# Performance work log

Hardware: AMD Instinct MI355X
Metric: run time of the kernel (lower is better)

## Reference

```python
import jax, jax.numpy as jnp
import numpy as np

G = 256          # voxel grid extent per axis
N = 30000        # number of active voxels
CHANNELS = [(4,16),(16,16),(16,32),(32,32),(32,32),(32,64),(64,64),(64,64),(64,64),(64,64),(64,64),(64,64),(64,128)]
BN_EPS = 1e-3

_OFFS = np.array([[i, j, k] for i in (-1, 0, 1) for j in (-1, 0, 1) for k in (-1, 0, 1)], dtype=np.int32)  # 27 kernel taps


def setup_inputs() -> dict:
    key = jax.random.key(0)
    ks = jax.random.split(key, 2 + len(CHANNELS))
    rng = np.random.default_rng(0)
    # unique active voxel coordinates in [0, G)^3
    c = rng.integers(0, G, size=(2 * N, 3))
    c = np.unique(c, axis=0)
    rng.shuffle(c)
    coords = jnp.asarray(c[:N], dtype=jnp.int32)
    inp = {
        "voxel_features": jax.random.normal(ks[0], (N, CHANNELS[0][0]), jnp.float32),
        "coords": coords,
    }
    for i, (ci, co) in enumerate(CHANNELS):
        inp[f"W{i}"] = jax.random.normal(ks[1 + i], (27, ci, co), jnp.float32) * (1.0 / np.sqrt(27.0 * ci))
        inp[f"g{i}"] = jnp.ones((co,), jnp.float32)
        inp[f"b{i}"] = jnp.zeros((co,), jnp.float32)
    return inp


def _neighbors(coords):
    """Build rulebook: for each of 27 taps, index of neighbor voxel (or masked)."""
    n = coords.shape[0]
    grid = jnp.full((G, G, G), -1, jnp.int32).at[coords[:, 0], coords[:, 1], coords[:, 2]].set(
        jnp.arange(n, dtype=jnp.int32))
    offs = jnp.asarray(_OFFS)
    nc = coords[None, :, :] + offs[:, None, :]               # [27, N, 3]
    inb = jnp.all((nc >= 0) & (nc < G), axis=-1)             # [27, N]
    ncc = jnp.clip(nc, 0, G - 1)
    nidx = grid[ncc[..., 0], ncc[..., 1], ncc[..., 2]]       # [27, N]
    valid = (inb & (nidx >= 0)).astype(jnp.float32)
    return jnp.maximum(nidx, 0), valid


def _sconv(feat, W, nidx, valid):
    # gather-GEMM: gathered [27, N, Cin] -> out [N, Cout]
    g = feat[nidx] * valid[..., None]
    return jnp.einsum('knc,kcd->nd', g, W)


def _bn_relu(x, g, b):
    m = jnp.mean(x, axis=0)
    v = jnp.var(x, axis=0)
    return jax.nn.relu((x - m) * jax.lax.rsqrt(v + BN_EPS) * g + b)


def reference(voxel_features, coords,
              W0, W1, W2, W3, W4, W5, W6, W7, W8, W9, W10, W11, W12,
              g0, g1, g2, g3, g4, g5, g6, g7, g8, g9, g10, g11, g12,
              b0, b1, b2, b3, b4, b5, b6, b7, b8, b9, b10, b11, b12):
    Ws = [W0, W1, W2, W3, W4, W5, W6, W7, W8, W9, W10, W11, W12]
    gs = [g0, g1, g2, g3, g4, g5, g6, g7, g8, g9, g10, g11, g12]
    bs = [b0, b1, b2, b3, b4, b5, b6, b7, b8, b9, b10, b11, b12]
    nidx, valid = _neighbors(coords)
    x = voxel_features
    for W, g, b in zip(Ws, gs, bs):
        x = _bn_relu(_sconv(x, W, nidx, valid), g, b)
    return x  # [N, 128] final backbone features
```

## Files before the change

### kernel.cpp

```cpp
#include <hip/hip_runtime.h>
#include <stdint.h>
#include <stddef.h>

#define GG 256
#define STP 16

typedef __attribute__((ext_vector_type(8))) short bf16x8;
typedef __attribute__((ext_vector_type(4))) float f32x4;

__device__ __forceinline__ float bf2f(short s) {
  return __builtin_bit_cast(float, ((unsigned)(unsigned short)s) << 16);
}
__device__ __forceinline__ short f2bf(float f) {
  unsigned u = __builtin_bit_cast(unsigned, f);
  unsigned r = (u + 0x7FFFu + ((u >> 16) & 1u)) >> 16;
  return (short)r;
}


__global__ __launch_bounds__(256) void k_clear_grid(uint32_t* g, int n32) {
  int i = blockIdx.x * 256 + threadIdx.x;
  int stride = gridDim.x * 256;
  for (; i < n32; i += stride) g[i] = 0xFFFFFFFFu;
}

__global__ __launch_bounds__(256) void k_scatter(const int* __restrict__ coords,
                                                 uint16_t* __restrict__ grid, int n) {
  int i = blockIdx.x * 256 + threadIdx.x;
  if (i >= n) return;
  int x = coords[3 * i], y = coords[3 * i + 1], z = coords[3 * i + 2];
  grid[(((x << 8) | y) << 8) | z] = (uint16_t)i;
}

__global__ __launch_bounds__(256) void k_rulebook(const int* __restrict__ coords,
                                                  const uint16_t* __restrict__ grid,
                                                  short* __restrict__ nidx, int n) {
  int i = blockIdx.x * 256 + threadIdx.x;
  if (i >= n) return;
  int x = coords[3 * i], y = coords[3 * i + 1], z = coords[3 * i + 2];
  int k = 0;
  for (int dx = -1; dx <= 1; ++dx)
    for (int dy = -1; dy <= 1; ++dy)
      for (int dz = -1; dz <= 1; ++dz) {
        int nx = x + dx, ny = y + dy, nz = z + dz;
        short v = -1;
        if (((nx | ny | nz) >= 0) && nx < GG && ny < GG && nz < GG) {
          uint16_t s = grid[(((nx << 8) | ny) << 8) | nz];
          if (s != 0xFFFFu) v = (short)s;
        }
        nidx[k * n + i] = v;
        ++k;
      }
}


__global__ __launch_bounds__(256) void k_zero(float* __restrict__ stats, float* __restrict__ zp) {
  int tot = 13 * 256 * STP;
  for (int i = blockIdx.x * 256 + threadIdx.x; i < tot; i += gridDim.x * 256) stats[i] = 0.0f;
  if (blockIdx.x == 0 && threadIdx.x < 64) zp[threadIdx.x] = 0.0f;
}


struct PackArgs {
  const float* W[13];
  short* P[13];
  int ci[13], co[13], nkb[13];
};

__global__ __launch_bounds__(256) void k_pack(PackArgs pa) {
  int L = blockIdx.y;
  int ci = pa.ci[L], co = pa.co[L], nkb = pa.nkb[L];
  int total = nkb * co * 32;
  const float* W = pa.W[L];
  short* P = pa.P[L];
  for (int e = blockIdx.x * 256 + threadIdx.x; e < total; e += gridDim.x * 256) {
    int kk = e & 31;
    int rest = e >> 5;
    int c = rest % co;
    int kb = rest / co;
    int k = kb * 32 + kk;
    int tap = k / ci, cc = k % ci;
    float v = (tap < 27) ? W[((size_t)tap * ci + cc) * co + c] : 0.0f;
    P[e] = f2bf(v);
  }
}


__global__ __launch_bounds__(256) void k_sconv_l0(const float* __restrict__ feat,
                                                  const float* __restrict__ W,
                                                  const short* __restrict__ nidx,
                                                  float* __restrict__ y,
                                                  float* __restrict__ stats, int n) {
  int i = blockIdx.x * 256 + threadIdx.x;
  bool act = i < n;
  int ii = act ? i : (n - 1);
  float acc[16];
#pragma unroll
  for (int c = 0; c < 16; ++c) acc[c] = 0.0f;
  for (int t = 0; t < 27; ++t) {
    int nid = nidx[t * n + ii];
    float4 f = make_float4(0.f, 0.f, 0.f, 0.f);
    if (act && nid >= 0) f = *(const float4*)(feat + 4 * (size_t)nid);
    const float* Wt = W + t * 64;
#pragma unroll
    for (int c = 0; c < 16; ++c)
      acc[c] = fmaf(f.x, Wt[c],
               fmaf(f.y, Wt[16 + c],
               fmaf(f.z, Wt[32 + c],
               fmaf(f.w, Wt[48 + c], acc[c]))));
  }
  if (act) {
    float* o = y + (size_t)i * 16;
#pragma unroll
    for (int c = 0; c < 16; c += 4) *(float4*)(o + c) = make_float4(acc[c], acc[c+1], acc[c+2], acc[c+3]);
  }
  __shared__ float ss[4][16], sq[4][16];
  int w = threadIdx.x >> 6, l = threadIdx.x & 63;
#pragma unroll
  for (int c = 0; c < 16; ++c) {
    float s = act ? acc[c] : 0.0f;
    float q = s * s;
#pragma unroll
    for (int off = 32; off; off >>= 1) {
      s += __shfl_xor(s, off);
      q += __shfl_xor(q, off);
    }
    if (l == 0) { ss[w][c] = s; sq[w][c] = q; }
  }
  __syncthreads();
  if (threadIdx.x < 16) {
    int c = threadIdx.x;
    atomicAdd(&stats[c * STP], ss[0][c] + ss[1][c] + ss[2][c] + ss[3][c]);
    atomicAdd(&stats[(16 + c) * STP], sq[0][c] + sq[1][c] + sq[2][c] + sq[3][c]);
  }
}


template <int CI, int CO>
__global__ __launch_bounds__(256) void k_sconv_mfma(
    const short* __restrict__ feat, const short* __restrict__ P,
    const short* __restrict__ nidx, int zoff,
    float* __restrict__ y, int n) {
  constexpr int NKB = (27 * CI + 31) / 32;
  constexpr int MT = (CO == 16) ? 4 : (CO == 32) ? 2 : 1;
  constexpr int WPM = 4 / MT;
  constexpr int NT = CO / (16 * WPM);
  constexpr int R = MT * 16;
  constexpr int PF = 4;

  const int w = threadIdx.x >> 6;
  const int l = threadIdx.x & 63;
  const int lo = l & 15, g = l >> 4;
  const int mt = w / WPM, nw = w % WPM;
  const int bvox = blockIdx.x * R;
  const int rowg = bvox + mt * 16 + lo;
  const int rowc = (rowg < n) ? rowg : (n - 1);

  int offs[28];
#pragma unroll
  for (int t = 0; t < 27; ++t) {
    int nid = (int)nidx[t * n + rowc];
    offs[t] = (nid >= 0) ? nid * (CI * 2) : zoff;
  }
  offs[27] = zoff;

  const int chb0 = (CI == 16) ? ((g & 1) * 16) : (g * 16);
  const char* fb = (const char*)feat + chb0;

  const char* pb[NT];
#pragma unroll
  for (int j = 0; j < NT; ++j)
    pb[j] = (const char*)P + (((nw + j * WPM) * 16 + lo) * 64 + g * 16);

  auto A = [&](int kb) -> bf16x8 {
    int off;
    if (CI == 64) {
      off = offs[kb >> 1] + ((kb & 1) << 6);
    } else if (CI == 32) {
      off = offs[kb];
    } else {
      int o0 = offs[2 * kb];
      int o1 = offs[2 * kb + 1];
      off = (g < 2) ? o0 : o1;
    }
    return *(const bf16x8*)(fb + off);
  };

  bf16x8 ab[PF];
  bf16x8 bb[PF][NT];
#pragma unroll
  for (int i = 0; i < PF; ++i) {
    ab[i] = A(i);
#pragma unroll
    for (int j = 0; j < NT; ++j)
      bb[i][j] = *(const bf16x8*)(pb[j] + (size_t)i * (CO * 64));
  }

  f32x4 acc[NT];
#pragma unroll
  for (int j = 0; j < NT; ++j) acc[j] = (f32x4){0.f, 0.f, 0.f, 0.f};

#pragma unroll
  for (int kb = 0; kb < NKB; ++kb) {
    bf16x8 a = ab[kb % PF];
    bf16x8 bcur[NT];
#pragma unroll
    for (int j = 0; j < NT; ++j) bcur[j] = bb[kb % PF][j];
    if (kb + PF < NKB) {
      ab[kb % PF] = A(kb + PF);
#pragma unroll
      for (int j = 0; j < NT; ++j)
        bb[kb % PF][j] = *(const bf16x8*)(pb[j] + (size_t)(kb + PF) * (CO * 64));
    }
#pragma unroll
    for (int j = 0; j < NT; ++j)
      acc[j] = __builtin_amdgcn_mfma_f32_16x16x32_bf16(a, bcur[j], acc[j], 0, 0, 0);
  }

  __shared__ float ys[R * CO];
#pragma unroll
  for (int j = 0; j < NT; ++j) {
    int col = (nw + j * WPM) * 16 + lo;
#pragma unroll
    for (int r = 0; r < 4; ++r)
      ys[(mt * 16 + 4 * g + r) * CO + col] = acc[j][r];
  }
  __syncthreads();
  constexpr int IT = (R * CO / 4) / 256;
#pragma unroll
  for (int e4 = 0; e4 < IT; ++e4) {
    int e = e4 * 256 + threadIdx.x;
    int gidx = bvox * CO + e * 4;
    if (gidx < n * CO) *(float4*)(y + gidx) = *(const float4*)(ys + e * 4);
  }
}


template <int CO>
__global__ __launch_bounds__(256) void k_stats(const float* __restrict__ y,
                                               float* __restrict__ stats, int n) {
  const int tid = threadIdx.x;
  const int c0 = (tid * 4) & (CO - 1);
  float s0 = 0.f, s1 = 0.f, s2 = 0.f, s3 = 0.f;
  float q0 = 0.f, q1 = 0.f, q2 = 0.f, q3 = 0.f;
  const int tot4 = n * CO / 4;
  for (int i = blockIdx.x * 256 + tid; i < tot4; i += gridDim.x * 256) {
    float4 v = *(const float4*)(y + (size_t)i * 4);
    s0 += v.x; q0 += v.x * v.x;
    s1 += v.y; q1 += v.y * v.y;
    s2 += v.z; q2 += v.z * v.z;
    s3 += v.w; q3 += v.w * v.w;
  }
  __shared__ float ps[2 * CO];
  for (int i = tid; i < 2 * CO; i += 256) ps[i] = 0.f;
  __syncthreads();
  atomicAdd(&ps[c0 + 0], s0);
  atomicAdd(&ps[c0 + 1], s1);
  atomicAdd(&ps[c0 + 2], s2);
  atomicAdd(&ps[c0 + 3], s3);
  atomicAdd(&ps[CO + c0 + 0], q0);
  atomicAdd(&ps[CO + c0 + 1], q1);
  atomicAdd(&ps[CO + c0 + 2], q2);
  atomicAdd(&ps[CO + c0 + 3], q3);
  __syncthreads();
  for (int c = tid; c < CO; c += 256) {
    atomicAdd(&stats[c * STP], ps[c]);
    atomicAdd(&stats[(CO + c) * STP], ps[CO + c]);
  }
}


template <int CO, bool OUTF32>
__global__ __launch_bounds__(256) void k_bn_apply(const float* __restrict__ yv,
                                                  const float* __restrict__ stats,
                                                  const float* __restrict__ gam,
                                                  const float* __restrict__ bet,
                                                  void* __restrict__ outv, int n) {
  int idx = blockIdx.x * 256 + threadIdx.x;
  int tot = n * CO / 8;
  if (idx >= tot) return;
  size_t e0 = (size_t)idx * 8;
  int c0 = (int)(e0 & (CO - 1));
  float invn = 1.0f / (float)n;

  const float4* p = (const float4*)(yv + e0);
  float4 u0 = p[0], u1 = p[1];
  float vin[8] = {u0.x, u0.y, u0.z, u0.w, u1.x, u1.y, u1.z, u1.w};

  float vout[8];
#pragma unroll
  for (int j = 0; j < 8; ++j) {
    int c = c0 + j;
    float m = stats[c * STP] * invn;
    float var = fmaf(-m, m, stats[(CO + c) * STP] * invn);
    float rstd = rsqrtf(var + 1e-3f);
    float o = fmaf((vin[j] - m) * rstd, gam[c], bet[c]);
    vout[j] = fmaxf(o, 0.0f);
  }

  if (OUTF32) {
    float4* q = (float4*)((float*)outv + e0);
    q[0] = make_float4(vout[0], vout[1], vout[2], vout[3]);
    q[1] = make_float4(vout[4], vout[5], vout[6], vout[7]);
  } else {
    bf16x8 o;
#pragma unroll
    for (int j = 0; j < 8; ++j) o[j] = f2bf(vout[j]);
    *(bf16x8*)((short*)outv + e0) = o;
  }
}


extern "C" void kernel_launch(void* const* d_in, const int* in_sizes, int n_in,
                              void* d_out, int out_size, void* d_ws, size_t ws_size,
                              hipStream_t stream) {
  const float* vf = (const float*)d_in[0];
  const int* coords = (const int*)d_in[1];
  const int n = in_sizes[1] / 3;

  static const int CIs[13] = {4, 16, 16, 32, 32, 32, 64, 64, 64, 64, 64, 64, 64};
  static const int COs[13] = {16, 16, 32, 32, 32, 64, 64, 64, 64, 64, 64, 64, 128};

  char* ws = (char*)d_ws;
  size_t off = 0;
  auto carve = [&](size_t bytes) { void* p = ws + off; off = (off + bytes + 255) & ~(size_t)255; return p; };
  uint16_t* grid = (uint16_t*)carve((size_t)GG * GG * GG * 2);
  short* nidx = (short*)carve((size_t)27 * n * 2);
  short* featA = (short*)carve((size_t)n * 128 * 2);
  short* featB = (short*)carve((size_t)n * 128 * 2);
  float* y = (float*)carve((size_t)n * 128 * 4);
  short* Ppool = (short*)carve((size_t)4 * 1024 * 1024);
  float* stats = (float*)carve((size_t)13 * 256 * STP * 4);
  float* zpage = (float*)carve(256);

  PackArgs pa;
  {
    size_t poff = 0;
    for (int L = 0; L < 13; ++L) {
      int ci = CIs[L], co = COs[L];
      int nkb = (27 * ci + 31) / 32;
      pa.W[L] = (const float*)d_in[2 + 3 * L];
      pa.P[L] = Ppool + poff;
      pa.ci[L] = ci; pa.co[L] = co; pa.nkb[L] = nkb;
      poff += (size_t)nkb * co * 32;
    }
  }

  const int n32 = GG * GG * GG / 2;
  k_clear_grid<<<2048, 256, 0, stream>>>((uint32_t*)grid, n32);
  k_scatter<<<(n + 255) / 256, 256, 0, stream>>>(coords, grid, n);
  k_rulebook<<<(n + 255) / 256, 256, 0, stream>>>(coords, grid, nidx, n);
  k_zero<<<208, 256, 0, stream>>>(stats, zpage);
  k_pack<<<dim3(128, 13), 256, 0, stream>>>(pa);

  k_sconv_l0<<<(n + 255) / 256, 256, 0, stream>>>(vf, pa.W[0], nidx, y, stats, n);
  k_bn_apply<16, false><<<((n * 16 / 8) + 255) / 256, 256, 0, stream>>>(
      y, stats, (const float*)d_in[3], (const float*)d_in[4], (void*)featA, n);

  short* cur = featA;
  short* nxt = featB;

#define RUN_MFMA(L, CI, CO, LAST)                                                             \
  do {                                                                                        \
    constexpr int MT_ = ((CO) == 16) ? 4 : ((CO) == 32) ? 2 : 1;                              \
    const int nblk = (n + MT_ * 16 - 1) / (MT_ * 16);                                         \
    float* st = stats + 256 * STP * (L);                                                      \
    int zoff = (int)((char*)zpage - (char*)cur);                                              \
    k_sconv_mfma<CI, CO><<<nblk, 256, 0, stream>>>(cur, (const short*)pa.P[L], nidx,          \
                                                   zoff, y, n);                               \
    k_stats<CO><<<256, 256, 0, stream>>>(y, st, n);                                           \
    const float* gg = (const float*)d_in[3 + 3 * (L)];                                        \
    const float* bb = (const float*)d_in[4 + 3 * (L)];                                        \
    int nb = ((n * (CO) / 8) + 255) / 256;                                                    \
    if (LAST) {                                                                               \
      k_bn_apply<CO, true><<<nb, 256, 0, stream>>>(y, st, gg, bb, (void*)d_out, n);           \
    } else {                                                                                  \
      k_bn_apply<CO, false><<<nb, 256, 0, stream>>>(y, st, gg, bb, (void*)nxt, n);            \
      short* t_ = cur; cur = nxt; nxt = t_;                                                   \
    }                                                                                         \
  } while (0)

  RUN_MFMA(1, 16, 16, false);
  RUN_MFMA(2, 16, 32, false);
  RUN_MFMA(3, 32, 32, false);
  RUN_MFMA(4, 32, 32, false);
  RUN_MFMA(5, 32, 64, false);
  RUN_MFMA(6, 64, 64, false);
  RUN_MFMA(7, 64, 64, false);
  RUN_MFMA(8, 64, 64, false);
  RUN_MFMA(9, 64, 64, false);
  RUN_MFMA(10, 64, 64, false);
  RUN_MFMA(11, 64, 64, false);
  RUN_MFMA(12, 64, 128, true);
#undef RUN_MFMA
}
```

Before: 794.7 us.

## Split K dimension across four waves with LDS reduction in sparse conv

The gather-GEMM kernel now gives each block 16 voxels instead of up to 64. The four waves split the 27-tap K dimension four ways, each covering all output columns, and their partial accumulators are summed through padded shared memory before the store. Packed weights are padded so each wave gets an equal K slice. This cuts per-thread tap offsets and shortens each wave's serial MFMA chain, aiming for more blocks and parallelism. The cost is four times as many blocks, redundant A-gathers per row group, and an extra LDS reduction step.

```diff
diff --git a/kernel.cpp b/kernel.cpp
--- a/kernel.cpp
+++ b/kernel.cpp
@@ -64,13 +64,13 @@
 struct PackArgs {
   const float* W[13];
   short* P[13];
-  int ci[13], co[13], nkb[13];
+  int ci[13], co[13], nkbp[13];
 };
 
 __global__ __launch_bounds__(256) void k_pack(PackArgs pa) {
   int L = blockIdx.y;
-  int ci = pa.ci[L], co = pa.co[L], nkb = pa.nkb[L];
-  int total = nkb * co * 32;
+  int ci = pa.ci[L], co = pa.co[L], nkbp = pa.nkbp[L];
+  int total = nkbp * co * 32;
   const float* W = pa.W[L];
   short* P = pa.P[L];
   for (int e = blockIdx.x * 256 + threadIdx.x; e < total; e += gridDim.x * 256) {
@@ -142,49 +142,44 @@
     const short* __restrict__ nidx, int zoff,
     float* __restrict__ y, int n) {
   constexpr int NKB = (27 * CI + 31) / 32;
-  constexpr int MT = (CO == 16) ? 4 : (CO == 32) ? 2 : 1;
-  constexpr int WPM = 4 / MT;
-  constexpr int NT = CO / (16 * WPM);
-  constexpr int R = MT * 16;
-  constexpr int PF = 4;
+  constexpr int KS = (NKB + 3) / 4;
+  constexpr int NT = CO / 16;
+  constexpr int TPW = (CI == 64) ? KS / 2 : (CI == 16) ? 2 * KS : KS;
+  static_assert(CI != 64 || (KS % 2 == 0), "CI=64 path assumes even KS (half-parity from local j)");
+  constexpr int PF = 2;
 
   const int w = threadIdx.x >> 6;
   const int l = threadIdx.x & 63;
   const int lo = l & 15, g = l >> 4;
-  const int mt = w / WPM, nw = w % WPM;
-  const int bvox = blockIdx.x * R;
-  const int rowg = bvox + mt * 16 + lo;
+  const int bvox = blockIdx.x * 16;
+  const int rowg = bvox + lo;
   const int rowc = (rowg < n) ? rowg : (n - 1);
 
-  int offs[28];
-#pragma unroll
-  for (int t = 0; t < 27; ++t) {
-    int nid = (int)nidx[t * n + rowc];
+  int offs[TPW];
+#pragma unroll
+  for (int t = 0; t < TPW; ++t) {
+    int tap = TPW * w + t;
+    int nid = (tap < 27) ? (int)nidx[tap * n + rowc] : -1;
     offs[t] = (nid >= 0) ? nid * (CI * 2) : zoff;
   }
-  offs[27] = zoff;
-
-  const int chb0 = (CI == 16) ? ((g & 1) * 16) : (g * 16);
-  const char* fb = (const char*)feat + chb0;
-
-  const char* pb[NT];
-#pragma unroll
-  for (int j = 0; j < NT; ++j)
-    pb[j] = (const char*)P + (((nw + j * WPM) * 16 + lo) * 64 + g * 16);
-
-  auto A = [&](int kb) -> bf16x8 {
+
+  const char* fb = (const char*)feat;
+  const char* pb = (const char*)P + (lo * 64 + g * 16) + (size_t)(w * KS) * (CO * 64);
+
+  auto A = [&](int j) -> bf16x8 {
     int off;
-    if (CI == 64) {
-      off = offs[kb >> 1] + ((kb & 1) << 6);
-    } else if (CI == 32) {
-      off = offs[kb];
-    } else {
-      int o0 = offs[2 * kb];
-      int o1 = offs[2 * kb + 1];
-      off = (g < 2) ? o0 : o1;
-    }
+    if (CI == 64)      off = offs[j >> 1] + ((j & 1) << 6) + g * 16;
+    else if (CI == 32) off = offs[j] + g * 16;
+    else               off = offs[2 * j + (g >> 1)] + (g & 1) * 16;
     return *(const bf16x8*)(fb + off);
   };
+  auto B = [&](int j, int t) -> bf16x8 {
+    return *(const bf16x8*)(pb + (size_t)j * (CO * 64) + t * 1024);
+  };
+
+  f32x4 acc[NT];
+#pragma unroll
+  for (int t = 0; t < NT; ++t) acc[t] = (f32x4){0.f, 0.f, 0.f, 0.f};
 
   bf16x8 ab[PF];
   bf16x8 bb[PF][NT];
@@ -192,46 +187,51 @@
   for (int i = 0; i < PF; ++i) {
     ab[i] = A(i);
 #pragma unroll
-    for (int j = 0; j < NT; ++j)
-      bb[i][j] = *(const bf16x8*)(pb[j] + (size_t)i * (CO * 64));
-  }
-
-  f32x4 acc[NT];
-#pragma unroll
-  for (int j = 0; j < NT; ++j) acc[j] = (f32x4){0.f, 0.f, 0.f, 0.f};
-
-#pragma unroll
-  for (int kb = 0; kb < NKB; ++kb) {
-    bf16x8 a = ab[kb % PF];
+    for (int t = 0; t < NT; ++t) bb[i][t] = B(i, t);
+  }
+
+#pragma unroll
+  for (int j = 0; j < KS; ++j) {
+    bf16x8 a = ab[j % PF];
     bf16x8 bcur[NT];
 #pragma unroll
-    for (int j = 0; j < NT; ++j) bcur[j] = bb[kb % PF][j];
-    if (kb + PF < NKB) {
-      ab[kb % PF] = A(kb + PF);
-#pragma unroll
-      for (int j = 0; j < NT; ++j)
-        bb[kb % PF][j] = *(const bf16x8*)(pb[j] + (size_t)(kb + PF) * (CO * 64));
+    for (int t = 0; t < NT; ++t) bcur[t] = bb[j % PF][t];
+    if (j + PF < KS) {
+      ab[j % PF] = A(j + PF);
+#pragma unroll
+      for (int t = 0; t < NT; ++t) bb[j % PF][t] = B(j + PF, t);
     }
 #pragma unroll
-    for (int j = 0; j < NT; ++j)
-      acc[j] = __builtin_amdgcn_mfma_f32_16x16x32_bf16(a, bcur[j], acc[j], 0, 0, 0);
-  }
-
-  __shared__ float ys[R * CO];
-#pragma unroll
-  for (int j = 0; j < NT; ++j) {
-    int col = (nw + j * WPM) * 16 + lo;
+    for (int t = 0; t < NT; ++t)
+      acc[t] = __builtin_amdgcn_mfma_f32_16x16x32_bf16(a, bcur[t], acc[t], 0, 0, 0);
+  }
+
+  constexpr int LDSP = CO + 4;
+  __shared__ float ps[4 * 16 * LDSP];
+#pragma unroll
+  for (int t = 0; t < NT; ++t) {
+    int col = 16 * t + lo;
 #pragma unroll
     for (int r = 0; r < 4; ++r)
-      ys[(mt * 16 + 4 * g + r) * CO + col] = acc[j][r];
+      ps[(w * 16 + 4 * g + r) * LDSP + col] = acc[t][r];
   }
   __syncthreads();
-  constexpr int IT = (R * CO / 4) / 256;
-#pragma unroll
-  for (int e4 = 0; e4 < IT; ++e4) {
-    int e = e4 * 256 + threadIdx.x;
-    int gidx = bvox * CO + e * 4;
-    if (gidx < n * CO) *(float4*)(y + gidx) = *(const float4*)(ys + e * 4);
+  constexpr int NF4 = 16 * CO / 4;
+#pragma unroll
+  for (int e0 = 0; e0 < NF4; e0 += 256) {
+    int e = e0 + threadIdx.x;
+    if (NF4 % 256 != 0 && e >= NF4) break;
+    int row = e / (CO / 4);
+    int c4 = e % (CO / 4);
+    float4 s = *(const float4*)&ps[(0 * 16 + row) * LDSP + 4 * c4];
+    const float4 s1 = *(const float4*)&ps[(1 * 16 + row) * LDSP + 4 * c4];
+    const float4 s2 = *(const float4*)&ps[(2 * 16 + row) * LDSP + 4 * c4];
+    const float4 s3 = *(const float4*)&ps[(3 * 16 + row) * LDSP + 4 * c4];
+    s.x += s1.x + s2.x + s3.x;
+    s.y += s1.y + s2.y + s3.y;
+    s.z += s1.z + s2.z + s3.z;
+    s.w += s1.w + s2.w + s3.w;
+    if (bvox + row < n) *(float4*)(y + (size_t)(bvox + row) * CO + 4 * c4) = s;
   }
 }
 
@@ -339,10 +339,12 @@
     for (int L = 0; L < 13; ++L) {
       int ci = CIs[L], co = COs[L];
       int nkb = (27 * ci + 31) / 32;
+      int ks = (nkb + 3) / 4;
+      int nkbp = 4 * ks;
       pa.W[L] = (const float*)d_in[2 + 3 * L];
       pa.P[L] = Ppool + poff;
-      pa.ci[L] = ci; pa.co[L] = co; pa.nkb[L] = nkb;
-      poff += (size_t)nkb * co * 32;
+      pa.ci[L] = ci; pa.co[L] = co; pa.nkbp[L] = nkbp;
+      poff += (size_t)nkbp * co * 32;
     }
   }
 
@@ -359,11 +361,10 @@
 
   short* cur = featA;
   short* nxt = featB;
+  const int nblk = (n + 15) / 16;
 
 #define RUN_MFMA(L, CI, CO, LAST)                                                             \
   do {                                                                                        \
-    constexpr int MT_ = ((CO) == 16) ? 4 : ((CO) == 32) ? 2 : 1;                              \
-    const int nblk = (n + MT_ * 16 - 1) / (MT_ * 16);                                         \
     float* st = stats + 256 * STP * (L);                                                      \
     int zoff = (int)((char*)zpage - (char*)cur);                                              \
     k_sconv_mfma<CI, CO><<<nblk, 256, 0, stream>>>(cur, (const short*)pa.P[L], nidx,          \
```

Result: faster. 724.6 us (-8.8%).
